# Kernel tuning notes

Hardware: AMD Instinct MI355X
Metric: run time of the kernel (lower is better)

Reference implementation:

```python
import jax, jax.numpy as jnp
import numpy as np

T, H, NH, NKV, HD, E, K, I = 1024, 2048, 16, 4, 128, 16, 2, 768
EPS = 1e-6
THETA = 10000.0


def setup_inputs() -> dict:
    key = jax.random.key(0)
    ks = jax.random.split(key, 8)
    s = 0.02
    return {
        "hidden_states": jax.random.normal(ks[0], (T, H), jnp.float32),
        "positions": jnp.arange(T, dtype=jnp.int32),
        "w_norm1": jnp.ones((H,), jnp.float32),
        "w_norm2": jnp.ones((H,), jnp.float32),
        "w_qkv": jax.random.normal(ks[1], (H, (NH + 2 * NKV) * HD), jnp.float32) * s,
        "w_qnorm": jnp.ones((HD,), jnp.float32),
        "w_knorm": jnp.ones((HD,), jnp.float32),
        "w_o": jax.random.normal(ks[2], (NH * HD, H), jnp.float32) * s,
        "w_router": jax.random.normal(ks[3], (H, E), jnp.float32) * s,
        "w_gate": jax.random.normal(ks[4], (E, H, I), jnp.float32) * s,
        "w_up": jax.random.normal(ks[5], (E, H, I), jnp.float32) * s,
        "w_down": jax.random.normal(ks[6], (E, I, H), jnp.float32) * s,
    }


def rmsnorm(x, w):
    return x * jax.lax.rsqrt(jnp.mean(x * x, axis=-1, keepdims=True) + EPS) * w


def apply_rope(x, positions):
    # NEOX-style rotary, full head_dim. x: [T, n_heads, HD]
    half = HD // 2
    inv_freq = 1.0 / (THETA ** (jnp.arange(half, dtype=jnp.float32) / half))
    ang = positions.astype(jnp.float32)[:, None] * inv_freq  # [T, half]
    cos = jnp.cos(ang)[:, None, :]
    sin = jnp.sin(ang)[:, None, :]
    x1, x2 = x[..., :half], x[..., half:]
    return jnp.concatenate([x1 * cos - x2 * sin, x2 * cos + x1 * sin], axis=-1)


def reference(hidden_states, positions, w_norm1, w_norm2, w_qkv, w_qnorm, w_knorm,
              w_o, w_router, w_gate, w_up, w_down):
    # prepare_attn: residual = x; h = input_layernorm(x)
    residual = hidden_states
    h = rmsnorm(hidden_states, w_norm1)

    # --- attention (bidirectional, GQA, per-head q/k RMSNorm + RoPE) ---
    qkv = h @ w_qkv
    q, k, v = jnp.split(qkv, [NH * HD, NH * HD + NKV * HD], axis=-1)
    q = rmsnorm(q.reshape(T, NH, HD), w_qnorm)
    k = rmsnorm(k.reshape(T, NKV, HD), w_knorm)
    v = v.reshape(T, NKV, HD)
    q = apply_rope(q, positions)
    k = apply_rope(k, positions)
    rep = NH // NKV
    kf = jnp.repeat(k, rep, axis=1)  # [T, NH, HD]
    vf = jnp.repeat(v, rep, axis=1)
    scores = jnp.einsum('tnd,snd->nts', q, kf) * (HD ** -0.5)  # [NH, T, T]
    p = jax.nn.softmax(scores, axis=-1)
    ctx = jnp.einsum('nts,snd->tnd', p, vf).reshape(T, NH * HD)
    attn_out = ctx @ w_o

    # prepare_mlp: residual = residual + attn_out; h = post_attention_layernorm(residual)
    residual = residual + attn_out
    h = rmsnorm(residual, w_norm2)

    # --- sparse MoE: softmax router, top-k renormalize, SwiGLU experts ---
    logits = h @ w_router
    probs = jax.nn.softmax(logits, axis=-1)
    topw, topi = jax.lax.top_k(probs, K)
    topw = topw / jnp.sum(topw, axis=-1, keepdims=True)
    gates = jnp.zeros((T, E), h.dtype).at[jnp.arange(T)[:, None], topi].set(topw)
    g = jnp.einsum('th,ehi->eti', h, w_gate)
    u = jnp.einsum('th,ehi->eti', h, w_up)
    y = jnp.einsum('eti,eih->eth', jax.nn.silu(g) * u, w_down)
    moe_out = jnp.einsum('eth,te->th', y, gates)

    return moe_out, residual
```

## Files before the change

### kernel.cpp

```cpp
#include <hip/hip_runtime.h>

#define T_    1024
#define H_    2048
#define NH_   16
#define NKV_  4
#define HD_   128
#define E_    16
#define I_    768
#define QKVN  3072

typedef __attribute__((ext_vector_type(8))) short  short8;
typedef __attribute__((ext_vector_type(4))) float  f32x4;
typedef unsigned short u16;

__device__ inline u16 f2bf(float f) {
  unsigned u = __builtin_bit_cast(unsigned, f);
  return (u16)((u + 0x7fffu + ((u >> 16) & 1u)) >> 16);
}
__device__ inline float bf2f(u16 h) {
  unsigned u = ((unsigned)h) << 16;
  return __builtin_bit_cast(float, u);
}

__device__ inline void gll16(const u16* g, u16* l) {
  __builtin_amdgcn_global_load_lds(
      (const __attribute__((address_space(1))) void*)g,
      (__attribute__((address_space(3))) void*)l, 16, 0, 0);
}
__device__ inline void gll16f(const float* g, float* l) {
  __builtin_amdgcn_global_load_lds(
      (const __attribute__((address_space(1))) void*)g,
      (__attribute__((address_space(3))) void*)l, 16, 0, 0);
}

__device__ inline float blk_sum(float v, float* lds) {
#pragma unroll
  for (int o = 32; o; o >>= 1) v += __shfl_down(v, o);
  int w = threadIdx.x >> 6;
  __syncthreads();
  if ((threadIdx.x & 63) == 0) lds[w] = v;
  __syncthreads();
  float s = lds[0];
  int nw = blockDim.x >> 6;
  for (int i = 1; i < nw; ++i) s += lds[i];
  return s;
}


__device__ inline void mma2F(const u16* As, const float* Bf, f32x4 acc[2][2]) {
  const int lane = threadIdx.x & 63, wv = threadIdx.x >> 6;
  const int wr = wv >> 1, wc = wv & 1;
  const int kk = (lane >> 4) * 8, rr = lane & 15;
  short8 aF[2], bF[2];
#pragma unroll
  for (int m = 0; m < 2; ++m)
    aF[m] = *(const short8*)(As + (wr * 32 + m * 16 + rr) * 32 + kk);
#pragma unroll
  for (int n = 0; n < 2; ++n) {
    int c = wc * 32 + n * 16 + rr;
    short8 b;
#pragma unroll
    for (int j = 0; j < 8; ++j)
      b[j] = (short)f2bf(Bf[(kk + j) * 64 + c]);
    bF[n] = b;
  }
#pragma unroll
  for (int m = 0; m < 2; ++m)
#pragma unroll
    for (int n = 0; n < 2; ++n)
      acc[m][n] = __builtin_amdgcn_mfma_f32_16x16x32_bf16(aF[m], bF[n], acc[m][n], 0, 0, 0);
}

#define ZERO_ACC(acc) do { \
  _Pragma("unroll") for (int m_ = 0; m_ < 2; ++m_) \
  _Pragma("unroll") for (int n_ = 0; n_ < 2; ++n_) acc[m_][n_] = (f32x4){0.f,0.f,0.f,0.f}; \
} while (0)

#define EPI_ROW(m, r)  (((threadIdx.x >> 6) >> 1) * 32 + (m)*16 + (((threadIdx.x&63) >> 4) * 4) + (r))
#define EPI_COL(n)     ((((threadIdx.x >> 6) & 1) * 32) + (n)*16 + ((threadIdx.x&63) & 15))

template<int NT, class IA, class IB>
__device__ inline void pipe3(IA ia, IB ib,
                             u16* A0, u16* A1, u16* A2,
                             float* B0, float* B1, float* B2,
                             f32x4 acc[2][2]) {
  ia(A0, 0); ib(B0, 0);
  ia(A1, 1); ib(B1, 1);
  ia(A2, 2); ib(B2, 2);
  u16 *a0 = A0, *a1 = A1, *a2 = A2;
  float *b0 = B0, *b1 = B1, *b2 = B2;
#pragma unroll 1
  for (int t = 0; t < NT; ++t) {
    int rem = NT - 1 - t;
    if (rem >= 2)      asm volatile("s_waitcnt vmcnt(4)" ::: "memory");
    else if (rem == 1) asm volatile("s_waitcnt vmcnt(2)" ::: "memory");
    else               asm volatile("s_waitcnt vmcnt(0)" ::: "memory");
    __builtin_amdgcn_s_barrier();
    mma2F(a0, b0, acc);
    __builtin_amdgcn_s_barrier();
    if (t + 3 < NT) { ia(a0, t + 3); ib(b0, t + 3); }
    u16* ta = a0; a0 = a1; a1 = a2; a2 = ta;
    float* tb = b0; b0 = b1; b1 = b2; b2 = tb;
  }
}


__global__ __launch_bounds__(256) void k_rms1(const float* x, const float* w, u16* out) {
  __shared__ float lds[4];
  int t = blockIdx.x, tid = threadIdx.x;
  float v[8]; float ss = 0.f;
#pragma unroll
  for (int i = 0; i < 8; ++i) { v[i] = x[(size_t)t * H_ + tid + 256 * i]; ss += v[i] * v[i]; }
  ss = blk_sum(ss, lds);
  float inv = rsqrtf(ss * (1.f / H_) + 1e-6f);
#pragma unroll
  for (int i = 0; i < 8; ++i)
    out[(size_t)t * H_ + tid + 256 * i] = f2bf(v[i] * inv * w[tid + 256 * i]);
}

__global__ __launch_bounds__(256) void k_rms2(const float* x, const float* w,
                                              float* outf, u16* outb) {
  __shared__ float lds[4];
  int t = blockIdx.x, tid = threadIdx.x;
  float v[8]; float ss = 0.f;
#pragma unroll
  for (int i = 0; i < 8; ++i) { v[i] = x[(size_t)t * H_ + tid + 256 * i]; ss += v[i] * v[i]; }
  ss = blk_sum(ss, lds);
  float inv = rsqrtf(ss * (1.f / H_) + 1e-6f);
#pragma unroll
  for (int i = 0; i < 8; ++i) {
    float r = v[i] * inv * w[tid + 256 * i];
    outf[(size_t)t * H_ + tid + 256 * i] = r;
    outb[(size_t)t * H_ + tid + 256 * i] = f2bf(r);
  }
}

__global__ __launch_bounds__(512) void k_qkv(const u16* h1, const float* wqkv, float* qkv) {
  __shared__ __align__(16) u16 A0[128 * 32], A1[128 * 32], A2[128 * 32];
  __shared__ __align__(16) float B0[32 * 64], B1[32 * 64], B2[32 * 64];
  int bn = blockIdx.x, bm = blockIdx.y, tid = threadIdx.x;
  f32x4 acc[2][2]; ZERO_ACC(acc);
  auto ia = [&](u16* As, int kt) {
    gll16(h1 + (size_t)(bm * 128 + (tid >> 2)) * H_ + kt * 32 + (tid & 3) * 8,
          As + (tid & 448) * 8);
  };
  auto ib = [&](float* Bf, int kt) {
    gll16f(wqkv + (size_t)(kt * 32 + (tid >> 4)) * QKVN + bn * 64 + (tid & 15) * 4,
           Bf + (tid & 448) * 4);
  };
  pipe3<H_ / 32>(ia, ib, A0, A1, A2, B0, B1, B2, acc);
#pragma unroll
  for (int m = 0; m < 2; ++m)
#pragma unroll
    for (int n = 0; n < 2; ++n) {
      f32x4 a = acc[m][n];
#pragma unroll
      for (int r = 0; r < 4; ++r)
        qkv[(size_t)(bm * 128 + EPI_ROW(m, r)) * QKVN + bn * 64 + EPI_COL(n)] = a[r];
    }
}

__global__ __launch_bounds__(256) void k_qkrope(const float* qkv, const int* pos,
                                                const float* wq, const float* wk,
                                                u16* q, u16* kk, u16* vT) {
  __shared__ float cs[64], sn[64];
  int t = blockIdx.x, tid = threadIdx.x, lane = tid & 63, w = tid >> 6;
  if (tid < 64) {
    float fr = expf(-((float)tid / 64.f) * 9.210340371976184f);
    float ang = (float)pos[t] * fr;
    float s_, c_; sincosf(ang, &s_, &c_);
    cs[tid] = c_; sn[tid] = s_;
  }
  __syncthreads();
  const float* row = qkv + (size_t)t * QKVN;
  for (int h = w; h < NH_; h += 4) {
    float x1 = row[h * 128 + lane], x2 = row[h * 128 + 64 + lane];
    float ss = x1 * x1 + x2 * x2;
#pragma unroll
    for (int o = 32; o; o >>= 1) ss += __shfl_down(ss, o);
    ss = __shfl(ss, 0);
    float inv = rsqrtf(ss * (1.f / HD_) + 1e-6f);
    float n1 = x1 * inv * wq[lane], n2 = x2 * inv * wq[64 + lane];
    float o1 = n1 * cs[lane] - n2 * sn[lane];
    float o2 = n2 * cs[lane] + n1 * sn[lane];
    q[(size_t)t * (NH_ * HD_) + h * 128 + lane] = f2bf(o1);
    q[(size_t)t * (NH_ * HD_) + h * 128 + 64 + lane] = f2bf(o2);
  }
  if (w < NKV_) {
    int h = w;
    float x1 = row[2048 + h * 128 + lane], x2 = row[2048 + h * 128 + 64 + lane];
    float ss = x1 * x1 + x2 * x2;
#pragma unroll
    for (int o = 32; o; o >>= 1) ss += __shfl_down(ss, o);
    ss = __shfl(ss, 0);
    float inv = rsqrtf(ss * (1.f / HD_) + 1e-6f);
    float n1 = x1 * inv * wk[lane], n2 = x2 * inv * wk[64 + lane];
    float o1 = n1 * cs[lane] - n2 * sn[lane];
    float o2 = n2 * cs[lane] + n1 * sn[lane];
    kk[((size_t)h * T_ + t) * HD_ + lane] = f2bf(o1);
    kk[((size_t)h * T_ + t) * HD_ + 64 + lane] = f2bf(o2);
    float v1 = row[2560 + h * 128 + lane], v2 = row[2560 + h * 128 + 64 + lane];
    vT[((size_t)(h * 128 + lane)) * T_ + t] = f2bf(v1);
    vT[((size_t)(h * 128 + 64 + lane)) * T_ + t] = f2bf(v2);
  }
}

__global__ __launch_bounds__(256) void k_fattn(const u16* q, const u16* kb,
                                               const u16* vT, float* opart, float* lpart) {
  __shared__ __align__(16) u16 Ks[64 * 136];
  __shared__ __align__(16) u16 Vs[128 * 72];
  __shared__ __align__(16) u16 Ps[4 * 16 * 72];
  int h = blockIdx.x, qt = blockIdx.y, kvs = blockIdx.z;
  int tid = threadIdx.x, lane = tid & 63, wv = tid >> 6;
  int rr = lane & 15, kk = (lane >> 4) * 8;
  const u16* kbh = kb + (size_t)(h >> 2) * T_ * HD_;
  const u16* vTh = vT + (size_t)(h >> 2) * HD_ * T_;
  int q0 = qt * 64 + wv * 16;
  short8 qf[4];
#pragma unroll
  for (int ks = 0; ks < 4; ++ks)
    qf[ks] = *(const short8*)(q + (size_t)(q0 + rr) * (NH_ * HD_) + h * 128 + ks * 32 + kk);
  f32x4 oacc[8];
#pragma unroll
  for (int i = 0; i < 8; ++i) oacc[i] = (f32x4){0.f, 0.f, 0.f, 0.f};
  float lsum[4] = {0.f, 0.f, 0.f, 0.f};
  const float scale = 0.08838834764831845f;
  u16* Pw = Ps + wv * 16 * 72;
#pragma unroll 1
  for (int kv = kvs * 4; kv < kvs * 4 + 4; ++kv) {
    __syncthreads();
    {
      uint4 kreg[4];
#pragma unroll
      for (int i = 0; i < 4; ++i) {
        int c = tid + 256 * i;
        kreg[i] = *(const uint4*)(kbh + (size_t)(kv * 64 + (c >> 4)) * HD_ + (c & 15) * 8);
      }
#pragma unroll
      for (int i = 0; i < 4; ++i) {
        int c = tid + 256 * i;
        *(uint4*)(Ks + (c >> 4) * 136 + (c & 15) * 8) = kreg[i];
      }
    }
    {
      uint4 vreg[4];
#pragma unroll
      for (int i = 0; i < 4; ++i) {
        int c = tid + 256 * i;
        vreg[i] = *(const uint4*)(vTh + (size_t)(c >> 3) * T_ + kv * 64 + (c & 7) * 8);
      }
#pragma unroll
      for (int i = 0; i < 4; ++i) {
        int c = tid + 256 * i;
        *(uint4*)(Vs + (c >> 3) * 72 + (c & 7) * 8) = vreg[i];
      }
    }
    __syncthreads();
    f32x4 sacc[4];
#pragma unroll
    for (int nf = 0; nf < 4; ++nf) sacc[nf] = (f32x4){0.f, 0.f, 0.f, 0.f};
#pragma unroll
    for (int ks = 0; ks < 4; ++ks)
#pragma unroll
      for (int nf = 0; nf < 4; ++nf) {
        short8 bF = *(const short8*)(Ks + (nf * 16 + rr) * 136 + ks * 32 + kk);
        sacc[nf] = __builtin_amdgcn_mfma_f32_16x16x32_bf16(qf[ks], bF, sacc[nf], 0, 0, 0);
      }
#pragma unroll
    for (int nf = 0; nf < 4; ++nf)
#pragma unroll
      for (int r = 0; r < 4; ++r) {
        float p = __expf(sacc[nf][r] * scale);
        lsum[r] += p;
        Pw[((lane >> 4) * 4 + r) * 72 + nf * 16 + rr] = f2bf(p);
      }
#pragma unroll
    for (int ks2 = 0; ks2 < 2; ++ks2) {
      short8 pa = *(const short8*)(Pw + rr * 72 + ks2 * 32 + kk);
#pragma unroll
      for (int nd = 0; nd < 8; ++nd) {
        short8 bV = *(const short8*)(Vs + (nd * 16 + rr) * 72 + ks2 * 32 + kk);
        oacc[nd] = __builtin_amdgcn_mfma_f32_16x16x32_bf16(pa, bV, oacc[nd], 0, 0, 0);
      }
    }
  }
#pragma unroll
  for (int r = 0; r < 4; ++r) {
#pragma unroll
    for (int o = 1; o < 16; o <<= 1) lsum[r] += __shfl_xor(lsum[r], o);
  }
  if ((lane & 15) == 0) {
#pragma unroll
    for (int r = 0; r < 4; ++r)
      lpart[((size_t)kvs * NH_ + h) * T_ + q0 + (lane >> 4) * 4 + r] = lsum[r];
  }
  float* op = opart + (size_t)kvs * T_ * (NH_ * HD_);
#pragma unroll
  for (int nd = 0; nd < 8; ++nd)
#pragma unroll
    for (int r = 0; r < 4; ++r)
      op[(size_t)(q0 + (lane >> 4) * 4 + r) * (NH_ * HD_) + h * 128 + nd * 16 + rr] =
          oacc[nd][r];
}

__global__ __launch_bounds__(256) void k_attnfin(const float* opart, const float* lpart,
                                                 u16* ctx) {
  int t = blockIdx.x, tid = threadIdx.x;
#pragma unroll
  for (int i = 0; i < 8; ++i) {
    int idx = tid + 256 * i;
    int h = idx >> 7;
    float l = 0.f, o = 0.f;
#pragma unroll
    for (int s = 0; s < 4; ++s) {
      l += lpart[((size_t)s * NH_ + h) * T_ + t];
      o += opart[(size_t)s * T_ * (NH_ * HD_) + (size_t)t * (NH_ * HD_) + idx];
    }
    ctx[(size_t)t * (NH_ * HD_) + idx] = f2bf(o / l);
  }
}

__global__ __launch_bounds__(512) void k_wo(const u16* ctx, const float* wo,
                                            const float* hs, float* resid) {
  __shared__ __align__(16) u16 A0[128 * 32], A1[128 * 32], A2[128 * 32];
  __shared__ __align__(16) float B0[32 * 64], B1[32 * 64], B2[32 * 64];
  int bn = blockIdx.x, bm = blockIdx.y, tid = threadIdx.x;
  f32x4 acc[2][2]; ZERO_ACC(acc);
  auto ia = [&](u16* As, int kt) {
    gll16(ctx + (size_t)(bm * 128 + (tid >> 2)) * H_ + kt * 32 + (tid & 3) * 8,
          As + (tid & 448) * 8);
  };
  auto ib = [&](float* Bf, int kt) {
    gll16f(wo + (size_t)(kt * 32 + (tid >> 4)) * H_ + bn * 64 + (tid & 15) * 4,
           Bf + (tid & 448) * 4);
  };
  pipe3<H_ / 32>(ia, ib, A0, A1, A2, B0, B1, B2, acc);
#pragma unroll
  for (int m = 0; m < 2; ++m)
#pragma unroll
    for (int n = 0; n < 2; ++n) {
      f32x4 a = acc[m][n];
#pragma unroll
      for (int r = 0; r < 4; ++r) {
        size_t idx = (size_t)(bm * 128 + EPI_ROW(m, r)) * H_ + bn * 64 + EPI_COL(n);
        resid[idx] = a[r] + hs[idx];
      }
    }
}

__global__ __launch_bounds__(256) void k_router(const float* h2f, const float* wr_,
                                                int* topi, float* topw, int* cnt) {
  __shared__ float xs[H_];
  __shared__ float red[4][16];
  __shared__ float lg[16];
  int t = blockIdx.x, tid = threadIdx.x;
#pragma unroll
  for (int i = 0; i < 8; ++i) xs[tid + 256 * i] = h2f[(size_t)t * H_ + tid + 256 * i];
  __syncthreads();
  int e = tid & 15, p = tid >> 4;
  float s = 0.f;
  int b0 = p * 128;
  for (int i = 0; i < 128; ++i) s += xs[b0 + i] * wr_[(size_t)(b0 + i) * E_ + e];
  s += __shfl_down(s, 32);
  s += __shfl_down(s, 16);
  int lane = tid & 63, w = tid >> 6;
  if (lane < 16) red[w][lane] = s;
  __syncthreads();
  if (tid < 16) lg[tid] = red[0][tid] + red[1][tid] + red[2][tid] + red[3][tid];
  __syncthreads();
  if (tid == 0) {
    float l1 = -1e30f; int e1 = 0;
    for (int i = 0; i < E_; ++i) if (lg[i] > l1) { l1 = lg[i]; e1 = i; }
    float l2 = -1e30f; int e2 = 0;
    for (int i = 0; i < E_; ++i) if (i != e1 && lg[i] > l2) { l2 = lg[i]; e2 = i; }
    float d = __expf(l2 - l1);
    float w1 = 1.f / (1.f + d), w2 = d / (1.f + d);
    topi[2 * t] = e1; topi[2 * t + 1] = e2;
    topw[2 * t] = w1; topw[2 * t + 1] = w2;
    atomicAdd(&cnt[e1], 1);
    atomicAdd(&cnt[e2], 1);
  }
}

__global__ void k_scan(const int* cnt, int* basearr) {
  if (threadIdx.x == 0) {
    int b = 0;
    for (int e = 0; e < E_; ++e) { basearr[e] = b; b += cnt[e]; }
    basearr[E_] = b;
  }
}

__global__ __launch_bounds__(256) void k_assign(const int* topi, const float* topw,
                                                const int* basearr, int* posc,
                                                int* tok, float* wslot) {
  int t = blockIdx.x * 256 + threadIdx.x;
  if (t < T_) {
#pragma unroll
    for (int j = 0; j < 2; ++j) {
      int e = topi[2 * t + j];
      int p = atomicAdd(&posc[e], 1);
      int s = basearr[e] + p;
      tok[s] = t;
      wslot[s] = topw[2 * t + j];
    }
  }
}

__global__ __launch_bounds__(512) void k_gateup(const u16* h2b,
                                                const float* wg, const float* wu,
                                                const int* cnt, const int* basearr, const int* tok,
                                                u16* act) {
  __shared__ __align__(16) u16 A0[128 * 32], A1[128 * 32], A2[128 * 32];
  __shared__ __align__(16) float B0[32 * 64], B1[32 * 64], B2[32 * 64];
  __shared__ int gat_s[128];
  int e = blockIdx.x;
  int c = cnt[e];
  int mt = blockIdx.z;
  if (mt * 128 >= c) return;
  int basee = basearr[e];
  int gmax = c - mt * 128;
  int n0 = blockIdx.y * 32;
  int tid = threadIdx.x;
  if (tid < 128) {
    int r = mt * 128 + tid;
    gat_s[tid] = (r < c) ? tok[basee + r] : tok[basee];
  }
  __syncthreads();
  int grow = gat_s[tid >> 2];
  const float* Bg = wg + (size_t)e * H_ * I_;
  const float* Bu = wu + (size_t)e * H_ * I_;
  f32x4 acc[2][2]; ZERO_ACC(acc);
  auto ia = [&](u16* As, int kt) {
    gll16(h2b + (size_t)grow * H_ + kt * 32 + (tid & 3) * 8, As + (tid & 448) * 8);
  };
  auto ib = [&](float* Bf, int kt) {
    int n4 = (tid & 15) * 4;
    int fn = n4 >> 4;
    const float* base = (fn & 1) ? Bu : Bg;
    int col = n0 + (fn >> 1) * 16 + (n4 & 15);
    gll16f(base + (size_t)(kt * 32 + (tid >> 4)) * I_ + col, Bf + (tid & 448) * 4);
  };
  pipe3<H_ / 32>(ia, ib, A0, A1, A2, B0, B1, B2, acc);
  int slot0 = basee + mt * 128;
  int col = n0 + ((tid >> 6) & 1) * 16 + ((tid & 63) & 15);
#pragma unroll
  for (int m = 0; m < 2; ++m) {
#pragma unroll
    for (int r = 0; r < 4; ++r) {
      int row = EPI_ROW(m, r);
      if (row >= gmax) continue;
      float g = acc[m][0][r], u = acc[m][1][r];
      float sg = g / (1.f + __expf(-g));
      act[(size_t)(slot0 + row) * I_ + col] = f2bf(sg * u);
    }
  }
}

__global__ __launch_bounds__(512) void k_down(const u16* act, const float* wd,
                                              const int* cnt, const int* basearr,
                                              const int* tok, const float* wslot,
                                              float* moe) {
  __shared__ __align__(16) u16 A0[128 * 32], A1[128 * 32], A2[128 * 32];
  __shared__ __align__(16) float B0[32 * 64], B1[32 * 64], B2[32 * 64];
  int e = blockIdx.y;
  int c = cnt[e];
  int mt = blockIdx.z;
  if (mt * 128 >= c) return;
  int basee = basearr[e];
  int gmax = c - mt * 128;
  int slot0 = basee + mt * 128;
  int n0 = blockIdx.x * 64;
  int tid = threadIdx.x;
  const u16* Ap = act + (size_t)slot0 * I_;
  const float* Bp = wd + (size_t)e * I_ * H_;
  f32x4 acc[2][2]; ZERO_ACC(acc);
  auto ia = [&](u16* As, int kt) {
    gll16(Ap + (size_t)(tid >> 2) * I_ + kt * 32 + (tid & 3) * 8, As + (tid & 448) * 8);
  };
  auto ib = [&](float* Bf, int kt) {
    gll16f(Bp + (size_t)(kt * 32 + (tid >> 4)) * H_ + n0 + (tid & 15) * 4,
           Bf + (tid & 448) * 4);
  };
  pipe3<I_ / 32>(ia, ib, A0, A1, A2, B0, B1, B2, acc);
#pragma unroll
  for (int m = 0; m < 2; ++m)
#pragma unroll
    for (int n = 0; n < 2; ++n) {
      f32x4 a = acc[m][n];
#pragma unroll
      for (int r = 0; r < 4; ++r) {
        int row = EPI_ROW(m, r);
        if (row >= gmax) continue;
        int col = EPI_COL(n);
        int slot = slot0 + row;
        float wgt = wslot[slot];
        int tk = tok[slot];
        atomicAdd(&moe[(size_t)tk * H_ + n0 + col], a[r] * wgt);
      }
    }
}

extern "C" void kernel_launch(void* const* d_in, const int* in_sizes, int n_in,
                              void* d_out, int out_size, void* d_ws, size_t ws_size,
                              hipStream_t stream) {
  const float* hs    = (const float*)d_in[0];
  const int*   pos   = (const int*)d_in[1];
  const float* wn1   = (const float*)d_in[2];
  const float* wn2   = (const float*)d_in[3];
  const float* wqkv  = (const float*)d_in[4];
  const float* wqn   = (const float*)d_in[5];
  const float* wkn   = (const float*)d_in[6];
  const float* wo    = (const float*)d_in[7];
  const float* wrt   = (const float*)d_in[8];
  const float* wg    = (const float*)d_in[9];
  const float* wu    = (const float*)d_in[10];
  const float* wd    = (const float*)d_in[11];
  float* out = (float*)d_out;
  float* moe_out = out;
  float* resid   = out + (size_t)T_ * H_;

  char* ws = (char*)d_ws;
  size_t off = 0;
  auto alloc = [&](size_t bytes) { size_t r = off; off = (off + bytes + 255) & ~(size_t)255; return r; };
  u16*   h1    = (u16*)  (ws + alloc((size_t)T_ * H_ * 2));
  float* qkv   = (float*)(ws + alloc((size_t)T_ * QKVN * 4));
  u16*   q     = (u16*)  (ws + alloc((size_t)T_ * NH_ * HD_ * 2));
  u16*   kb    = (u16*)  (ws + alloc((size_t)NKV_ * T_ * HD_ * 2));
  u16*   vT    = (u16*)  (ws + alloc((size_t)NKV_ * HD_ * T_ * 2));
  u16*   ctx   = (u16*)  (ws + alloc((size_t)T_ * NH_ * HD_ * 2));
  float* opart = (float*)(ws + alloc((size_t)4 * T_ * NH_ * HD_ * 4));
  float* lpart = (float*)(ws + alloc((size_t)4 * NH_ * T_ * 4));
  float* h2f   = (float*)(ws + alloc((size_t)T_ * H_ * 4));
  u16*   h2b   = (u16*)  (ws + alloc((size_t)T_ * H_ * 2));
  u16*   act   = (u16*)  (ws + alloc((size_t)(2 * T_ + 256) * I_ * 2));
  int*   topi  = (int*)  (ws + alloc((size_t)T_ * 2 * 4));
  float* topw  = (float*)(ws + alloc((size_t)T_ * 2 * 4));
  int*   cnt   = (int*)  (ws + alloc(32 * 4));
  int*   posc  = cnt + 16;
  int*   base  = (int*)  (ws + alloc(32 * 4));
  int*   tok   = (int*)  (ws + alloc((size_t)(2 * T_ + 128) * 4));
  float* wsl   = (float*)(ws + alloc((size_t)(2 * T_ + 128) * 4));
  (void)ws_size; (void)in_sizes; (void)n_in; (void)out_size;

  hipMemsetAsync(moe_out, 0, (size_t)T_ * H_ * 4, stream);
  hipMemsetAsync(cnt, 0, 32 * 4, stream);

  k_rms1<<<T_, 256, 0, stream>>>(hs, wn1, h1);
  k_qkv<<<dim3(QKVN / 64, T_ / 128), 512, 0, stream>>>(h1, wqkv, qkv);
  k_qkrope<<<T_, 256, 0, stream>>>(qkv, pos, wqn, wkn, q, kb, vT);
  k_fattn<<<dim3(NH_, T_ / 64, 4), 256, 0, stream>>>(q, kb, vT, opart, lpart);
  k_attnfin<<<T_, 256, 0, stream>>>(opart, lpart, ctx);
  k_wo<<<dim3(H_ / 64, T_ / 128), 512, 0, stream>>>(ctx, wo, hs, resid);
  k_rms2<<<T_, 256, 0, stream>>>(resid, wn2, h2f, h2b);
  k_router<<<T_, 256, 0, stream>>>(h2f, wrt, topi, topw, cnt);
  k_scan<<<1, 64, 0, stream>>>(cnt, base);
  k_assign<<<4, 256, 0, stream>>>(topi, topw, base, posc, tok, wsl);
  k_gateup<<<dim3(E_, I_ / 32, T_ / 128), 512, 0, stream>>>(h2b, wg, wu, cnt, base, tok, act);
  k_down<<<dim3(H_ / 64, E_, T_ / 128), 512, 0, stream>>>(act, wd, cnt, base, tok, wsl, moe_out);
}
```

Measured before the change: 369.0 us.

## Deepen GEMM pipeline to four stages and convert B tile to bf16 once

Every fp32-weight GEMM now uses a four-deep async load pipeline instead of three. Each k-step, all threads cooperatively convert the fp32 B tile to a padded, transposed bf16 LDS buffer once, so the MFMA fragment load becomes a single vector read. Before, each wave did redundant scalar fp32 loads and conversions per fragment. This costs an extra barrier per step and more LDS per block, which may lower occupancy.

```diff
diff --git a/kernel.cpp b/kernel.cpp
--- a/kernel.cpp
+++ b/kernel.cpp
@@ -47,23 +47,18 @@
 }
 
 
-__device__ inline void mma2F(const u16* As, const float* Bf, f32x4 acc[2][2]) {
+template<int SA, int SB>
+__device__ inline void mma2(const u16* As, const u16* Bs, f32x4 acc[2][2]) {
   const int lane = threadIdx.x & 63, wv = threadIdx.x >> 6;
   const int wr = wv >> 1, wc = wv & 1;
   const int kk = (lane >> 4) * 8, rr = lane & 15;
   short8 aF[2], bF[2];
 #pragma unroll
   for (int m = 0; m < 2; ++m)
-    aF[m] = *(const short8*)(As + (wr * 32 + m * 16 + rr) * 32 + kk);
-#pragma unroll
-  for (int n = 0; n < 2; ++n) {
-    int c = wc * 32 + n * 16 + rr;
-    short8 b;
-#pragma unroll
-    for (int j = 0; j < 8; ++j)
-      b[j] = (short)f2bf(Bf[(kk + j) * 64 + c]);
-    bF[n] = b;
-  }
+    aF[m] = *(const short8*)(As + (wr * 32 + m * 16 + rr) * SA + kk);
+#pragma unroll
+  for (int n = 0; n < 2; ++n)
+    bF[n] = *(const short8*)(Bs + (wc * 32 + n * 16 + rr) * SB + kk);
 #pragma unroll
   for (int m = 0; m < 2; ++m)
 #pragma unroll
@@ -79,30 +74,57 @@
 #define EPI_ROW(m, r)  (((threadIdx.x >> 6) >> 1) * 32 + (m)*16 + (((threadIdx.x&63) >> 4) * 4) + (r))
 #define EPI_COL(n)     ((((threadIdx.x >> 6) & 1) * 32) + (n)*16 + ((threadIdx.x&63) & 15))
 
+template<class IA, class IB>
+__device__ inline void step4g(IA& ia, IB& ib, int t, int NT,
+                              u16* As, float* Fs, u16* Bb, f32x4 acc[2][2]) {
+  int rem = NT - 1 - t;
+  if (rem >= 3)      asm volatile("s_waitcnt vmcnt(6)" ::: "memory");
+  else if (rem == 2) asm volatile("s_waitcnt vmcnt(4)" ::: "memory");
+  else if (rem == 1) asm volatile("s_waitcnt vmcnt(2)" ::: "memory");
+  else               asm volatile("s_waitcnt vmcnt(0)" ::: "memory");
+  __builtin_amdgcn_s_barrier();
+  {
+    int cn = threadIdx.x & 63, ck = (threadIdx.x >> 6) * 4;
+    float f0 = Fs[(ck + 0) * 64 + cn];
+    float f1 = Fs[(ck + 1) * 64 + cn];
+    float f2 = Fs[(ck + 2) * 64 + cn];
+    float f3 = Fs[(ck + 3) * 64 + cn];
+    uint2 w;
+    w.x = (unsigned)f2bf(f0) | ((unsigned)f2bf(f1) << 16);
+    w.y = (unsigned)f2bf(f2) | ((unsigned)f2bf(f3) << 16);
+    *(uint2*)(Bb + cn * 40 + ck) = w;
+  }
+  asm volatile("s_waitcnt lgkmcnt(0)" ::: "memory");
+  __builtin_amdgcn_s_barrier();
+  mma2<32, 40>(As, Bb, acc);
+  asm volatile("" ::: "memory");
+  __builtin_amdgcn_s_barrier();
+  asm volatile("" ::: "memory");
+  if (t + 4 < NT) { ia(As, t + 4); ib(Fs, t + 4); }
+}
+
 template<int NT, class IA, class IB>
-__device__ inline void pipe3(IA ia, IB ib,
-                             u16* A0, u16* A1, u16* A2,
-                             float* B0, float* B1, float* B2,
-                             f32x4 acc[2][2]) {
-  ia(A0, 0); ib(B0, 0);
-  ia(A1, 1); ib(B1, 1);
-  ia(A2, 2); ib(B2, 2);
-  u16 *a0 = A0, *a1 = A1, *a2 = A2;
-  float *b0 = B0, *b1 = B1, *b2 = B2;
+__device__ inline void pipe4g(IA ia, IB ib,
+                              u16* A0, u16* A1, u16* A2, u16* A3,
+                              float* F0, float* F1, float* F2, float* F3,
+                              u16* Bb, f32x4 acc[2][2]) {
+  ia(A0, 0); ib(F0, 0);
+  ia(A1, 1); ib(F1, 1);
+  ia(A2, 2); ib(F2, 2);
+  ia(A3, 3); ib(F3, 3);
 #pragma unroll 1
-  for (int t = 0; t < NT; ++t) {
-    int rem = NT - 1 - t;
-    if (rem >= 2)      asm volatile("s_waitcnt vmcnt(4)" ::: "memory");
-    else if (rem == 1) asm volatile("s_waitcnt vmcnt(2)" ::: "memory");
-    else               asm volatile("s_waitcnt vmcnt(0)" ::: "memory");
-    __builtin_amdgcn_s_barrier();
-    mma2F(a0, b0, acc);
-    __builtin_amdgcn_s_barrier();
-    if (t + 3 < NT) { ia(a0, t + 3); ib(b0, t + 3); }
-    u16* ta = a0; a0 = a1; a1 = a2; a2 = ta;
-    float* tb = b0; b0 = b1; b1 = b2; b2 = tb;
-  }
-}
+  for (int t = 0; t < NT; t += 4) {
+    step4g(ia, ib, t,     NT, A0, F0, Bb, acc);
+    step4g(ia, ib, t + 1, NT, A1, F1, Bb, acc);
+    step4g(ia, ib, t + 2, NT, A2, F2, Bb, acc);
+    step4g(ia, ib, t + 3, NT, A3, F3, Bb, acc);
+  }
+}
+
+#define GEMM_LDS \
+  __shared__ __align__(16) u16 A0[128 * 32], A1[128 * 32], A2[128 * 32], A3[128 * 32]; \
+  __shared__ __align__(16) float F0[32 * 64], F1[32 * 64], F2[32 * 64], F3[32 * 64]; \
+  __shared__ __align__(16) u16 Bb[64 * 40];
 
 
 __global__ __launch_bounds__(256) void k_rms1(const float* x, const float* w, u16* out) {
@@ -136,8 +158,7 @@
 }
 
 __global__ __launch_bounds__(512) void k_qkv(const u16* h1, const float* wqkv, float* qkv) {
-  __shared__ __align__(16) u16 A0[128 * 32], A1[128 * 32], A2[128 * 32];
-  __shared__ __align__(16) float B0[32 * 64], B1[32 * 64], B2[32 * 64];
+  GEMM_LDS
   int bn = blockIdx.x, bm = blockIdx.y, tid = threadIdx.x;
   f32x4 acc[2][2]; ZERO_ACC(acc);
   auto ia = [&](u16* As, int kt) {
@@ -148,7 +169,7 @@
     gll16f(wqkv + (size_t)(kt * 32 + (tid >> 4)) * QKVN + bn * 64 + (tid & 15) * 4,
            Bf + (tid & 448) * 4);
   };
-  pipe3<H_ / 32>(ia, ib, A0, A1, A2, B0, B1, B2, acc);
+  pipe4g<H_ / 32>(ia, ib, A0, A1, A2, A3, F0, F1, F2, F3, Bb, acc);
 #pragma unroll
   for (int m = 0; m < 2; ++m)
 #pragma unroll
@@ -322,8 +343,7 @@
 
 __global__ __launch_bounds__(512) void k_wo(const u16* ctx, const float* wo,
                                             const float* hs, float* resid) {
-  __shared__ __align__(16) u16 A0[128 * 32], A1[128 * 32], A2[128 * 32];
-  __shared__ __align__(16) float B0[32 * 64], B1[32 * 64], B2[32 * 64];
+  GEMM_LDS
   int bn = blockIdx.x, bm = blockIdx.y, tid = threadIdx.x;
   f32x4 acc[2][2]; ZERO_ACC(acc);
   auto ia = [&](u16* As, int kt) {
@@ -334,7 +354,7 @@
     gll16f(wo + (size_t)(kt * 32 + (tid >> 4)) * H_ + bn * 64 + (tid & 15) * 4,
            Bf + (tid & 448) * 4);
   };
-  pipe3<H_ / 32>(ia, ib, A0, A1, A2, B0, B1, B2, acc);
+  pipe4g<H_ / 32>(ia, ib, A0, A1, A2, A3, F0, F1, F2, F3, Bb, acc);
 #pragma unroll
   for (int m = 0; m < 2; ++m)
 #pragma unroll
@@ -410,8 +430,7 @@
                                                 const float* wg, const float* wu,
                                                 const int* cnt, const int* basearr, const int* tok,
                                                 u16* act) {
-  __shared__ __align__(16) u16 A0[128 * 32], A1[128 * 32], A2[128 * 32];
-  __shared__ __align__(16) float B0[32 * 64], B1[32 * 64], B2[32 * 64];
+  GEMM_LDS
   __shared__ int gat_s[128];
   int e = blockIdx.x;
   int c = cnt[e];
@@ -440,7 +459,7 @@
     int col = n0 + (fn >> 1) * 16 + (n4 & 15);
     gll16f(base + (size_t)(kt * 32 + (tid >> 4)) * I_ + col, Bf + (tid & 448) * 4);
   };
-  pipe3<H_ / 32>(ia, ib, A0, A1, A2, B0, B1, B2, acc);
+  pipe4g<H_ / 32>(ia, ib, A0, A1, A2, A3, F0, F1, F2, F3, Bb, acc);
   int slot0 = basee + mt * 128;
   int col = n0 + ((tid >> 6) & 1) * 16 + ((tid & 63) & 15);
 #pragma unroll
@@ -460,8 +479,7 @@
                                               const int* cnt, const int* basearr,
                                               const int* tok, const float* wslot,
                                               float* moe) {
-  __shared__ __align__(16) u16 A0[128 * 32], A1[128 * 32], A2[128 * 32];
-  __shared__ __align__(16) float B0[32 * 64], B1[32 * 64], B2[32 * 64];
+  GEMM_LDS
   int e = blockIdx.y;
   int c = cnt[e];
   int mt = blockIdx.z;
@@ -481,7 +499,7 @@
     gll16f(Bp + (size_t)(kt * 32 + (tid >> 4)) * H_ + n0 + (tid & 15) * 4,
            Bf + (tid & 448) * 4);
   };
-  pipe3<I_ / 32>(ia, ib, A0, A1, A2, B0, B1, B2, acc);
+  pipe4g<I_ / 32>(ia, ib, A0, A1, A2, A3, F0, F1, F2, F3, Bb, acc);
 #pragma unroll
   for (int m = 0; m < 2; ++m)
 #pragma unroll
```

New measurement: 350.8 us. 1.05x faster.
